# Kernel optimization log

Measured on AMD Instinct MI355X. Metric: run time of the kernel, lower is better.

Reference implementation:

```python
import jax, jax.numpy as jnp
import numpy as np
import math

B, L, D_IN, D, H, NL, FF = 8, 1024, 32, 512, 8, 6, 64
DK = D // H

def _ln(x, g, b, eps=1e-5):
    m = jnp.mean(x, axis=-1, keepdims=True)
    v = jnp.mean((x - m) ** 2, axis=-1, keepdims=True)
    return (x - m) * jax.lax.rsqrt(v + eps) * g + b

def setup_inputs() -> dict:
    key = jax.random.key(0)
    ks = jax.random.split(key, 32)
    def nrm(k, shape, s=0.02):
        return jax.random.normal(k, shape, jnp.float32) * s
    x = jax.random.normal(ks[0], (B, L, D_IN), jnp.float32)
    mask = jnp.broadcast_to(jnp.tril(jnp.ones((L, L), jnp.int32))[None], (B, L, L))
    obs_time = jnp.arange(B * L, dtype=jnp.float32).reshape(B, L)
    inp = {
        "x": x, "mask": mask, "obs_time": obs_time,
        # embedding MLP: Linear(d_input,d) -> ReLU -> [Dropout] -> LayerNorm -> Linear(d,d)
        "emb_w1": nrm(ks[1], (D_IN, D)), "emb_b1": jnp.zeros((D,), jnp.float32),
        "emb_g": jnp.ones((D,), jnp.float32), "emb_beta": jnp.zeros((D,), jnp.float32),
        "emb_w2": nrm(ks[2], (D, D)), "emb_b2": jnp.zeros((D,), jnp.float32),
        # per-layer stacked params [NL, ...]
        "wq": nrm(ks[3], (NL, D, D)), "wk": nrm(ks[4], (NL, D, D)), "wv": nrm(ks[5], (NL, D, D)),
        "wo": nrm(ks[6], (NL, D, D)), "bo": jnp.zeros((NL, D), jnp.float32),
        "fw1": nrm(ks[7], (NL, D, FF)), "fb1": jnp.zeros((NL, FF), jnp.float32),
        "fw2": nrm(ks[8], (NL, FF, D)), "fb2": jnp.zeros((NL, D), jnp.float32),
        "g1": jnp.ones((NL, D), jnp.float32), "b1": jnp.zeros((NL, D), jnp.float32),
        "g2": jnp.ones((NL, D), jnp.float32), "b2": jnp.zeros((NL, D), jnp.float32),
    }
    return inp

def reference(x, mask, obs_time, emb_w1, emb_b1, emb_g, emb_beta, emb_w2, emb_b2,
              wq, wk, wv, wo, bo, fw1, fb1, fw2, fb2, g1, b1, g2, b2):
    # positional encoding: pe[...,0::2]=sin(t*div), pe[...,1::2]=cos(t*div)
    t = obs_time[..., None]  # [B,L,1]
    div = jnp.exp(jnp.arange(0, D, 2, dtype=jnp.float32) * (-math.log(10000.0) / D))
    pe = jnp.stack([jnp.sin(t * div), jnp.cos(t * div)], axis=-1).reshape(x.shape[0], x.shape[1], D)

    # embedding MLP (dropout = identity at eval)
    h = jax.nn.relu(x @ emb_w1 + emb_b1)
    h = _ln(h, emb_g, emb_beta)
    h = h @ emb_w2 + emb_b2
    h = h + pe

    Bx, Lx = h.shape[0], h.shape[1]
    scale = 1.0 / np.sqrt(DK).astype(np.float32)
    mask4 = (mask == 0)[:, None]  # [B,1,L,L]
    for i in range(NL):
        # self-attention
        q = (h @ wq[i]).reshape(Bx, Lx, H, DK).transpose(0, 2, 1, 3)  # bhld
        k = (h @ wk[i]).reshape(Bx, Lx, H, DK).transpose(0, 2, 1, 3)
        v = (h @ wv[i]).reshape(Bx, Lx, H, DK).transpose(0, 2, 1, 3)
        scores = jnp.einsum('bhqd,bhkd->bhqk', q, k) * scale
        scores = jnp.where(mask4, -jnp.inf, scores)
        attn = jax.nn.softmax(scores, axis=-1)
        o = jnp.einsum('bhqk,bhkd->bhqd', attn, v).transpose(0, 2, 1, 3).reshape(Bx, Lx, D)
        o = o @ wo[i] + bo[i]
        h = _ln(h + o, g1[i], b1[i])
        # feed-forward d -> 64 -> d
        f = jax.nn.relu(h @ fw1[i] + fb1[i]) @ fw2[i] + fb2[i]
        h = _ln(h + f, g2[i], b2[i])
    return h
```

## Files before the change

kernel.cpp:

```cpp
#include <hip/hip_runtime.h>
#include <math.h>

typedef unsigned short u16;
typedef unsigned int   u32;
typedef __bf16 bf16_t;
typedef bf16_t bf16x8 __attribute__((ext_vector_type(8)));
typedef float  f32x4  __attribute__((ext_vector_type(4)));
typedef u16    u16x8  __attribute__((ext_vector_type(8)));
typedef u16    u16x4  __attribute__((ext_vector_type(4)));

#define B_   8
#define L_   1024
#define DIN_ 32
#define D_   512
#define H_   8
#define NL_  6
#define FF_  64
#define M_   (B_*L_)
#define DD_  (D_*D_)

#define PE_COEF (-0.017988946039015984f)
#define SC2     (0.18033688011112042f)

__device__ __forceinline__ u16 f2bf(float f) {
  u32 u = __builtin_bit_cast(u32, f);
  u32 r = (u + 0x7FFFu + ((u >> 16) & 1u)) >> 16;
  return (u16)r;
}
__device__ __forceinline__ u16 f2bf_fast(float f) {
  u32 u = __builtin_bit_cast(u32, f);
  return (u16)((u + 0x8000u) >> 16);
}
__device__ __forceinline__ float bf2f(u16 v) {
  u32 u = ((u32)v) << 16;
  return __builtin_bit_cast(float, u);
}

#define GLOAD_LDS16(gp, lp) \
  __builtin_amdgcn_global_load_lds((const __attribute__((address_space(1))) u32*)(gp), \
                                   (__attribute__((address_space(3))) u32*)(lp), 16, 0, 0)

__global__ __launch_bounds__(256) void transpose_all(const float* __restrict__ wq, const float* __restrict__ wk,
                                                     const float* __restrict__ wv, const float* __restrict__ wo,
                                                     const float* __restrict__ ew2,
                                                     u16* __restrict__ qkvt, u16* __restrict__ wot,
                                                     u16* __restrict__ ew2t) {
  __shared__ float tile[32][33];
  int z = blockIdx.z;
  const float* src;
  u16* dst;
  if (z < 18) {
    int grp = z / 6, i = z % 6;
    src = (grp == 0 ? wq : grp == 1 ? wk : wv) + (size_t)i*DD_;
    dst = qkvt + (size_t)i*3*DD_ + (size_t)grp*DD_;
  } else if (z < 24) {
    int i = z - 18;
    src = wo + (size_t)i*DD_;
    dst = wot + (size_t)i*DD_;
  } else {
    src = ew2; dst = ew2t;
  }
  int k0 = blockIdx.y * 32, n0 = blockIdx.x * 32;
  int tx = threadIdx.x & 31, ty = threadIdx.x >> 5;
  #pragma unroll
  for (int i = 0; i < 4; ++i)
    tile[ty + i*8][tx] = src[(size_t)(k0 + ty + i*8)*512 + n0 + tx];
  __syncthreads();
  #pragma unroll
  for (int i = 0; i < 4; ++i)
    dst[(size_t)(n0 + ty + i*8)*512 + k0 + tx] = f2bf(tile[tx][ty + i*8]);
}

__global__ __launch_bounds__(256) void transpose_k(const float* __restrict__ W, u16* __restrict__ Wt,
                                                   int K, int N, size_t in_zs, size_t out_zs) {
  __shared__ float tile[32][33];
  size_t mi = (size_t)blockIdx.z * in_zs;
  size_t mo = (size_t)blockIdx.z * out_zs;
  int k0 = blockIdx.y * 32, n0 = blockIdx.x * 32;
  int tx = threadIdx.x & 31, ty = threadIdx.x >> 5;
  #pragma unroll
  for (int i = 0; i < 4; ++i)
    tile[ty + i*8][tx] = W[mi + (size_t)(k0 + ty + i*8)*N + n0 + tx];
  __syncthreads();
  #pragma unroll
  for (int i = 0; i < 4; ++i)
    Wt[mo + (size_t)(n0 + ty + i*8)*K + k0 + tx] = f2bf(tile[tx][ty + i*8]);
}

__global__ __launch_bounds__(256) void emb1_ln_kernel(const float* __restrict__ x, const float* __restrict__ W1,
                               const float* __restrict__ b1, const float* __restrict__ g,
                               const float* __restrict__ beta, u16* __restrict__ outb) {
  __shared__ float xs[DIN_];
  __shared__ float red[4];
  int m = blockIdx.x;
  int tid = threadIdx.x;
  if (tid < DIN_) xs[tid] = x[m*DIN_ + tid];
  __syncthreads();
  float v[2];
  #pragma unroll
  for (int r = 0; r < 2; ++r) {
    int n = tid + r*256;
    float acc = b1[n];
    #pragma unroll
    for (int k = 0; k < DIN_; ++k) acc += xs[k] * W1[k*D_ + n];
    v[r] = fmaxf(acc, 0.f);
  }
  float s = v[0] + v[1];
  #pragma unroll
  for (int off = 32; off > 0; off >>= 1) s += __shfl_down(s, off, 64);
  int wid = tid >> 6;
  if ((tid & 63) == 0) red[wid] = s;
  __syncthreads();
  float mean = (red[0] + red[1] + red[2] + red[3]) * (1.f/D_);
  float d0 = v[0] - mean, d1 = v[1] - mean;
  float vv = d0*d0 + d1*d1;
  #pragma unroll
  for (int off = 32; off > 0; off >>= 1) vv += __shfl_down(vv, off, 64);
  __syncthreads();
  if ((tid & 63) == 0) red[wid] = vv;
  __syncthreads();
  float var = (red[0] + red[1] + red[2] + red[3]) * (1.f/D_);
  float rstd = rsqrtf(var + 1e-5f);
  outb[(size_t)m*D_ + tid]       = f2bf(d0*rstd*g[tid]       + beta[tid]);
  outb[(size_t)m*D_ + tid + 256] = f2bf(d1*rstd*g[tid + 256] + beta[tid + 256]);
}

__global__ __launch_bounds__(256) void add_ln_kernel(const float* __restrict__ hin, const u16* __restrict__ res,
                              const float* __restrict__ g, const float* __restrict__ b,
                              float* __restrict__ outf, u16* __restrict__ outb) {
  int w = threadIdx.x >> 6, lane = threadIdx.x & 63;
  int m = blockIdx.x * 4 + w;
  const float* hr = hin + (size_t)m*D_;
  const u16*   rr = res + (size_t)m*D_;
  float v[8];
  float s = 0.f;
  #pragma unroll
  for (int i = 0; i < 8; ++i) {
    int c = lane + i*64;
    v[i] = hr[c] + bf2f(rr[c]);
    s += v[i];
  }
  #pragma unroll
  for (int off = 32; off > 0; off >>= 1) s += __shfl_xor(s, off, 64);
  float mean = s * (1.f/D_);
  float vs = 0.f;
  #pragma unroll
  for (int i = 0; i < 8; ++i) { v[i] -= mean; vs += v[i]*v[i]; }
  #pragma unroll
  for (int off = 32; off > 0; off >>= 1) vs += __shfl_xor(vs, off, 64);
  float rstd = rsqrtf(vs * (1.f/D_) + 1e-5f);
  #pragma unroll
  for (int i = 0; i < 8; ++i) {
    int c = lane + i*64;
    float o = v[i]*rstd*g[c] + b[c];
    outf[(size_t)m*D_ + c] = o;
    outb[(size_t)m*D_ + c] = f2bf(o);
  }
}

template<int BM, int BN, int EPI, bool WF, bool WB>
__global__ __launch_bounds__(256) void mgemm(const u16* __restrict__ A, const u16* __restrict__ Bt,
                            const float* __restrict__ bias, const float* __restrict__ extra,
                            float* __restrict__ Cf, u16* __restrict__ Cb,
                            int M, int N, int K) {
  constexpr int BK = 64;
  constexpr int AI = BM/32, BI = BN/32;
  __shared__ __align__(16) u16 As[2][BM*BK];
  __shared__ __align__(16) u16 Bs[2][BN*BK];
  const int WR = BM/2, WC = BN/2, MR = WR/16, NR = WC/16;
  int nx = gridDim.x;
  int nwg = nx * gridDim.y;
  int flat = blockIdx.y * nx + blockIdx.x;
  int wid = (flat & 7) * (nwg >> 3) + (flat >> 3);
  int bm = (wid / nx) * BM, bn = (wid % nx) * BN;
  int tid = threadIdx.x, w = tid >> 6, l = tid & 63;
  int wr = w >> 1, wc = w & 1;
  int lq = l & 15, lg = l >> 4;
  int lrow8 = l >> 3, lcol8 = l & 7;
  f32x4 acc[MR][NR];
  #pragma unroll
  for (int m = 0; m < MR; ++m)
    #pragma unroll
    for (int n = 0; n < NR; ++n) acc[m][n] = f32x4{0.f,0.f,0.f,0.f};

  auto stage = [&](int t, int bi) {
    int k0 = t * BK;
    #pragma unroll
    for (int i = 0; i < AI; ++i) {
      int row = (i*4 + w)*8 + lrow8;
      int c8 = lcol8 ^ ((row & 1) << 2);
      GLOAD_LDS16(A + (size_t)(bm + row)*K + k0 + c8*8, &As[bi][(i*4 + w)*512]);
    }
    #pragma unroll
    for (int i = 0; i < BI; ++i) {
      int row = (i*4 + w)*8 + lrow8;
      int c8 = lcol8 ^ ((row & 1) << 2);
      GLOAD_LDS16(Bt + (size_t)(bn + row)*K + k0 + c8*8, &Bs[bi][(i*4 + w)*512]);
    }
  };

  int nk = K / BK;
  stage(0, 0);
  asm volatile("s_waitcnt vmcnt(0)" ::: "memory");
  __builtin_amdgcn_s_barrier();
  __builtin_amdgcn_sched_barrier(0);

  int xh = lq & 1;
  #pragma unroll 1
  for (int t = 0; t < nk; ++t) {
    int buf = t & 1;
    if (t + 1 < nk) stage(t + 1, buf ^ 1);
    bf16x8 af[MR][2], bf[NR][2];
    #pragma unroll
    for (int m = 0; m < MR; ++m)
      #pragma unroll
      for (int h = 0; h < 2; ++h)
        af[m][h] = *(const bf16x8*)&As[buf][(wr*WR + m*16 + lq)*BK + (h ^ xh)*32 + lg*8];
    #pragma unroll
    for (int n = 0; n < NR; ++n)
      #pragma unroll
      for (int h = 0; h < 2; ++h)
        bf[n][h] = *(const bf16x8*)&Bs[buf][(wc*WC + n*16 + lq)*BK + (h ^ xh)*32 + lg*8];
    #pragma unroll
    for (int m = 0; m < MR; ++m)
      #pragma unroll
      for (int n = 0; n < NR; ++n) {
        acc[m][n] = __builtin_amdgcn_mfma_f32_16x16x32_bf16(af[m][0], bf[n][0], acc[m][n], 0, 0, 0);
        acc[m][n] = __builtin_amdgcn_mfma_f32_16x16x32_bf16(af[m][1], bf[n][1], acc[m][n], 0, 0, 0);
      }
    if (t + 1 < nk) {
      asm volatile("s_waitcnt vmcnt(0)" ::: "memory");
      __builtin_amdgcn_s_barrier();
      __builtin_amdgcn_sched_barrier(0);
    }
  }

  #pragma unroll
  for (int m = 0; m < MR; ++m) {
    #pragma unroll
    for (int n = 0; n < NR; ++n) {
      #pragma unroll
      for (int r = 0; r < 4; ++r) {
        int row = bm + wr*WR + m*16 + lg*4 + r;
        int col = bn + wc*WC + n*16 + lq;
        float v = acc[m][n][r];
        if (EPI & 1) v += bias[col];
        if (EPI & 2) v = fmaxf(v, 0.f);
        if (EPI & 4) {
          float fr  = __expf((float)(col & ~1) * PE_COEF);
          float arg = extra[row] * fr;
          v += (col & 1) ? cosf(arg) : sinf(arg);
        }
        if (WF) Cf[(size_t)row*N + col] = v;
        if (WB) Cb[(size_t)row*N + col] = f2bf(v);
      }
    }
  }
}

#define QS_ 1536
__global__ __launch_bounds__(256) void attn_kernel(const u16* __restrict__ Q, const u16* __restrict__ Kp,
                                                   const u16* __restrict__ V, u16* __restrict__ O) {
  __shared__ __align__(16) u16 Ks[2][64*72];
  __shared__ __align__(16) u16 Vt[2][64*72];
  __shared__ __align__(16) u16 Ps[4][16*72];
  int flat = blockIdx.y * 8 + blockIdx.x;
  int wid  = (flat & 7) * 64 + (flat >> 3);
  int pair = wid & 7, bh = wid >> 3;
  int b = bh >> 3, hh = bh & 7;
  int rowbase = b * L_, col0 = hh * 64;
  int tid = threadIdx.x, w = tid >> 6, l = tid & 63;
  int lq = l & 15, lg = l >> 4;

  int krow = tid >> 3, kseg = tid & 7;
  int vg = tid >> 5, vd2 = (tid & 31) * 2;

  u16x8 kr0, kr1;
  u32 vr[8];
  u16x8 oc16;
  #pragma unroll
  for (int i = 0; i < 8; ++i) oc16[i] = 0x3F80u;
  const bf16x8 onesA = __builtin_bit_cast(bf16x8, oc16);

  #define LOADKV(t) { \
    kr0 = *(const u16x8*)&Kp[(size_t)(rowbase + (t)*64 + krow)*QS_ + col0 + kseg*8]; \
    kr1 = *(const u16x8*)&Kp[(size_t)(rowbase + (t)*64 + krow + 32)*QS_ + col0 + kseg*8]; \
    _Pragma("unroll") \
    for (int i_ = 0; i_ < 8; ++i_) \
      vr[i_] = *(const u32*)&V[(size_t)(rowbase + (t)*64 + vg*8 + i_)*QS_ + col0 + vd2]; }

  LOADKV(0);

  #pragma unroll 1
  for (int half = 0; half < 2; ++half) {
    int qt = half ? (15 - pair) : pair;
    int qrow = rowbase + qt*64 + w*16 + lq;
    bf16x8 qa0 = *(const bf16x8*)&Q[(size_t)qrow*QS_ + col0 + lg*8];
    bf16x8 qa1 = *(const bf16x8*)&Q[(size_t)qrow*QS_ + col0 + 32 + lg*8];
    float m_s[4];
    f32x4 o[4], o4;
    #pragma unroll
    for (int r = 0; r < 4; ++r) m_s[r] = -1e30f;
    #pragma unroll
    for (int n = 0; n < 4; ++n) o[n] = f32x4{0.f,0.f,0.f,0.f};
    o4 = f32x4{0.f,0.f,0.f,0.f};

    #pragma unroll 1
    for (int kt = 0; kt <= qt; ++kt) {
      int buf = kt & 1;
      __syncthreads();
      *(u16x8*)&Ks[buf][krow*72 + kseg*8]        = kr0;
      *(u16x8*)&Ks[buf][(krow + 32)*72 + kseg*8] = kr1;
      {
        u16x8 vlo, vhi;
        #pragma unroll
        for (int i = 0; i < 8; ++i) { vlo[i] = (u16)(vr[i] & 0xffffu); vhi[i] = (u16)(vr[i] >> 16); }
        *(u16x8*)&Vt[buf][vd2*72 + vg*8]     = vlo;
        *(u16x8*)&Vt[buf][(vd2+1)*72 + vg*8] = vhi;
      }
      __syncthreads();
      int nt = (kt < qt) ? (kt + 1) : (half == 0 ? 0 : -1);
      if (nt >= 0) LOADKV(nt);

      f32x4 t4[4];
      __builtin_amdgcn_s_setprio(1);
      #pragma unroll
      for (int f = 0; f < 4; ++f) {
        bf16x8 k0 = *(const bf16x8*)&Ks[buf][(f*16 + lq)*72 + lg*8];
        bf16x8 k1 = *(const bf16x8*)&Ks[buf][(f*16 + lq)*72 + 32 + lg*8];
        f32x4 z = f32x4{0.f,0.f,0.f,0.f};
        z = __builtin_amdgcn_mfma_f32_16x16x32_bf16(qa0, k0, z, 0, 0, 0);
        z = __builtin_amdgcn_mfma_f32_16x16x32_bf16(qa1, k1, z, 0, 0, 0);
        #pragma unroll
        for (int r = 0; r < 4; ++r) t4[f][r] = z[r] * SC2;
      }
      __builtin_amdgcn_s_setprio(0);
      if (kt == qt) {
        #pragma unroll
        for (int f = 0; f < 4; ++f) {
          int kvg = f*16 + lq;
          #pragma unroll
          for (int r = 0; r < 4; ++r)
            if (kvg > w*16 + lg*4 + r) t4[f][r] = -1e30f;
        }
      }
      float tm[4];
      bool need = false;
      #pragma unroll
      for (int r = 0; r < 4; ++r) {
        float v = fmaxf(fmaxf(t4[0][r], t4[1][r]), fmaxf(t4[2][r], t4[3][r]));
        v = fmaxf(v, __shfl_xor(v, 1));
        v = fmaxf(v, __shfl_xor(v, 2));
        v = fmaxf(v, __shfl_xor(v, 4));
        v = fmaxf(v, __shfl_xor(v, 8));
        tm[r] = v;
        need = need || (v > m_s[r]);
      }
      if (__any(need)) {
        float corr[4];
        #pragma unroll
        for (int r = 0; r < 4; ++r) {
          float mn = fmaxf(m_s[r], tm[r]);
          corr[r] = __builtin_amdgcn_exp2f(m_s[r] - mn);
          m_s[r] = mn;
        }
        int bsrc = (lq >> 2)*16 + lq;
        float c0 = __shfl(corr[0], bsrc);
        float c1 = __shfl(corr[1], bsrc);
        float c2 = __shfl(corr[2], bsrc);
        float c3 = __shfl(corr[3], bsrc);
        float cb = (lq & 2) ? ((lq & 1) ? c3 : c2) : ((lq & 1) ? c1 : c0);
        #pragma unroll
        for (int n = 0; n < 4; ++n)
          #pragma unroll
          for (int r = 0; r < 4; ++r) o[n][r] *= cb;
        #pragma unroll
        for (int r = 0; r < 4; ++r) o4[r] *= cb;
      }
      #pragma unroll
      for (int r = 0; r < 4; ++r) {
        int prow = (lg*4 + r)*72;
        Ps[w][prow + lq]      = f2bf_fast(__builtin_amdgcn_exp2f(t4[0][r] - m_s[r]));
        Ps[w][prow + 16 + lq] = f2bf_fast(__builtin_amdgcn_exp2f(t4[1][r] - m_s[r]));
        Ps[w][prow + 32 + lq] = f2bf_fast(__builtin_amdgcn_exp2f(t4[2][r] - m_s[r]));
        Ps[w][prow + 48 + lq] = f2bf_fast(__builtin_amdgcn_exp2f(t4[3][r] - m_s[r]));
      }
      bf16x8 pB0 = *(const bf16x8*)&Ps[w][lq*72 + lg*8];
      bf16x8 pB1 = *(const bf16x8*)&Ps[w][lq*72 + 32 + lg*8];
      __builtin_amdgcn_s_setprio(1);
      o4 = __builtin_amdgcn_mfma_f32_16x16x32_bf16(onesA, pB0, o4, 0, 0, 0);
      o4 = __builtin_amdgcn_mfma_f32_16x16x32_bf16(onesA, pB1, o4, 0, 0, 0);
      #pragma unroll
      for (int n = 0; n < 4; ++n) {
        bf16x8 vA0 = *(const bf16x8*)&Vt[buf][(n*16 + lq)*72 + lg*8];
        bf16x8 vA1 = *(const bf16x8*)&Vt[buf][(n*16 + lq)*72 + 32 + lg*8];
        o[n] = __builtin_amdgcn_mfma_f32_16x16x32_bf16(vA0, pB0, o[n], 0, 0, 0);
        o[n] = __builtin_amdgcn_mfma_f32_16x16x32_bf16(vA1, pB1, o[n], 0, 0, 0);
      }
      __builtin_amdgcn_s_setprio(0);
    }
    float inv = 1.f / o4[0];
    #pragma unroll
    for (int n = 0; n < 4; ++n) {
      u16x4 pk;
      #pragma unroll
      for (int r = 0; r < 4; ++r) pk[r] = f2bf(o[n][r] * inv);
      *(u16x4*)&O[(size_t)(rowbase + qt*64 + w*16 + lq)*D_ + col0 + n*16 + lg*4] = pk;
    }
  }
  #undef LOADKV
}

extern "C" void kernel_launch(void* const* d_in, const int* in_sizes, int n_in,
                              void* d_out, int out_size, void* d_ws, size_t ws_size,
                              hipStream_t stream) {
  (void)in_sizes; (void)n_in; (void)out_size; (void)ws_size;
  const float* x      = (const float*)d_in[0];
  const float* obs    = (const float*)d_in[2];
  const float* emb_w1 = (const float*)d_in[3];
  const float* emb_b1 = (const float*)d_in[4];
  const float* emb_g  = (const float*)d_in[5];
  const float* emb_be = (const float*)d_in[6];
  const float* emb_w2 = (const float*)d_in[7];
  const float* emb_b2 = (const float*)d_in[8];
  const float* wq  = (const float*)d_in[9];
  const float* wk  = (const float*)d_in[10];
  const float* wv  = (const float*)d_in[11];
  const float* wo  = (const float*)d_in[12];
  const float* bo  = (const float*)d_in[13];
  const float* fw1 = (const float*)d_in[14];
  const float* fb1 = (const float*)d_in[15];
  const float* fw2 = (const float*)d_in[16];
  const float* fb2 = (const float*)d_in[17];
  const float* g1  = (const float*)d_in[18];
  const float* b1  = (const float*)d_in[19];
  const float* g2  = (const float*)d_in[20];
  const float* b2  = (const float*)d_in[21];
  float* out = (float*)d_out;

  float* hf  = (float*)d_ws;
  u16* hb    = (u16*)(hf + (size_t)M_*D_);
  u16* qkvb  = hb + (size_t)M_*D_;
  u16* ob    = qkvb + (size_t)M_*3*D_;
  u16* ofb   = ob + (size_t)M_*D_;
  u16* fhb   = ofb + (size_t)M_*D_;
  u16* qkvt  = fhb + (size_t)M_*FF_;
  u16* wot   = qkvt + (size_t)18*DD_;
  u16* ew2t  = wot + (size_t)6*DD_;
  u16* fw1t  = ew2t + (size_t)DD_;
  u16* fw2t  = fw1t + (size_t)6*D_*FF_;

  transpose_all<<<dim3(16,16,25), 256, 0, stream>>>(wq, wk, wv, wo, emb_w2, qkvt, wot, ew2t);
  transpose_k<<<dim3(2,16,6),  256, 0, stream>>>(fw1, fw1t, 512,  64, (size_t)D_*FF_, (size_t)D_*FF_);
  transpose_k<<<dim3(16,2,6),  256, 0, stream>>>(fw2, fw2t,  64, 512, (size_t)D_*FF_, (size_t)D_*FF_);

  emb1_ln_kernel<<<M_, 256, 0, stream>>>(x, emb_w1, emb_b1, emb_g, emb_be, ob);
  mgemm<128,128,5,true,true><<<dim3(4,64), 256, 0, stream>>>(ob, ew2t, emb_b2, obs, hf, hb, M_, D_, D_);

  for (int i = 0; i < NL_; ++i) {
    mgemm<128,128,0,false,true><<<dim3(12,64), 256, 0, stream>>>(hb, qkvt + (size_t)i*3*DD_,
        nullptr, nullptr, nullptr, qkvb, M_, 3*D_, D_);
    attn_kernel<<<dim3(8, B_*H_), 256, 0, stream>>>(qkvb, qkvb + D_, qkvb + 2*D_, ob);
    mgemm<128,128,1,false,true><<<dim3(4,64), 256, 0, stream>>>(ob, wot + (size_t)i*DD_,
        bo + i*D_, nullptr, nullptr, ofb, M_, D_, D_);
    add_ln_kernel<<<M_/4, 256, 0, stream>>>(hf, ofb, g1 + i*D_, b1 + i*D_, hf, hb);
    mgemm<64,64,3,false,true><<<dim3(1,128), 256, 0, stream>>>(hb, fw1t + (size_t)i*D_*FF_,
        fb1 + i*FF_, nullptr, nullptr, fhb, M_, FF_, D_);
    mgemm<128,128,1,false,true><<<dim3(4,64), 256, 0, stream>>>(fhb, fw2t + (size_t)i*D_*FF_,
        fb2 + i*D_, nullptr, nullptr, ofb, M_, D_, FF_);
    add_ln_kernel<<<M_/4, 256, 0, stream>>>(hf, ofb, g2 + i*D_, b2 + i*D_,
        (i == NL_-1) ? out : hf, hb);
  }
}
```

Baseline: 866.7 us.

## Fuse FFN with residual LayerNorm, triple-buffer GEMM, and prefetch attention K/V

The FFN block's two GEMMs, ReLU, bias, residual add and LayerNorm are replaced by one fused kernel. Each block of it handles 32 rows, keeps the 64-wide hidden activation in LDS and reads the weights straight from global memory. The generic GEMM moves from a double-buffered BK=64 loop to a triple-buffered BK=32 pipeline with partial vmcnt waits, and the XOR swizzle is dropped. The attention kernel now writes the next K/V tile to LDS at the end of each iteration, removing one barrier per tile. Together these cut launches and the round trips for the FFN intermediate and its output, at the cost of possible LDS bank conflicts and lower weight reuse in the fused FFN.

```diff
diff --git a/kernel.cpp b/kernel.cpp
--- a/kernel.cpp
+++ b/kernel.cpp
@@ -163,10 +163,10 @@
                             const float* __restrict__ bias, const float* __restrict__ extra,
                             float* __restrict__ Cf, u16* __restrict__ Cb,
                             int M, int N, int K) {
-  constexpr int BK = 64;
-  constexpr int AI = BM/32, BI = BN/32;
-  __shared__ __align__(16) u16 As[2][BM*BK];
-  __shared__ __align__(16) u16 Bs[2][BN*BK];
+  constexpr int NBUF = 3;
+  constexpr int LPT = BM/64 + BN/64;
+  __shared__ __align__(16) u16 As[NBUF][BM*32];
+  __shared__ __align__(16) u16 Bs[NBUF][BN*32];
   const int WR = BM/2, WC = BN/2, MR = WR/16, NR = WC/16;
   int nx = gridDim.x;
   int nwg = nx * gridDim.y;
@@ -176,63 +176,58 @@
   int tid = threadIdx.x, w = tid >> 6, l = tid & 63;
   int wr = w >> 1, wc = w & 1;
   int lq = l & 15, lg = l >> 4;
-  int lrow8 = l >> 3, lcol8 = l & 7;
   f32x4 acc[MR][NR];
   #pragma unroll
   for (int m = 0; m < MR; ++m)
     #pragma unroll
     for (int n = 0; n < NR; ++n) acc[m][n] = f32x4{0.f,0.f,0.f,0.f};
 
+  int srow = w*16 + (l >> 2);
+  int scol = (l & 3)*8;
+
   auto stage = [&](int t, int bi) {
-    int k0 = t * BK;
-    #pragma unroll
-    for (int i = 0; i < AI; ++i) {
-      int row = (i*4 + w)*8 + lrow8;
-      int c8 = lcol8 ^ ((row & 1) << 2);
-      GLOAD_LDS16(A + (size_t)(bm + row)*K + k0 + c8*8, &As[bi][(i*4 + w)*512]);
-    }
-    #pragma unroll
-    for (int i = 0; i < BI; ++i) {
-      int row = (i*4 + w)*8 + lrow8;
-      int c8 = lcol8 ^ ((row & 1) << 2);
-      GLOAD_LDS16(Bt + (size_t)(bn + row)*K + k0 + c8*8, &Bs[bi][(i*4 + w)*512]);
-    }
+    int k0 = t << 5;
+    #pragma unroll
+    for (int i = 0; i < BM/64; ++i)
+      GLOAD_LDS16(A + (size_t)(bm + i*64 + srow)*K + k0 + scol, &As[bi][i*2048 + w*512]);
+    #pragma unroll
+    for (int i = 0; i < BN/64; ++i)
+      GLOAD_LDS16(Bt + (size_t)(bn + i*64 + srow)*K + k0 + scol, &Bs[bi][i*2048 + w*512]);
   };
 
-  int nk = K / BK;
+  int nk = K >> 5;
   stage(0, 0);
-  asm volatile("s_waitcnt vmcnt(0)" ::: "memory");
-  __builtin_amdgcn_s_barrier();
-  __builtin_amdgcn_sched_barrier(0);
-
-  int xh = lq & 1;
+  if (nk > 1) stage(1, 1);
+  int bi = 0;
   #pragma unroll 1
   for (int t = 0; t < nk; ++t) {
-    int buf = t & 1;
-    if (t + 1 < nk) stage(t + 1, buf ^ 1);
-    bf16x8 af[MR][2], bf[NR][2];
+    if (t + 1 < nk) {
+      if constexpr (LPT == 2)      asm volatile("s_waitcnt vmcnt(2)" ::: "memory");
+      else if constexpr (LPT == 3) asm volatile("s_waitcnt vmcnt(3)" ::: "memory");
+      else if constexpr (LPT == 4) asm volatile("s_waitcnt vmcnt(4)" ::: "memory");
+      else                         asm volatile("s_waitcnt vmcnt(0)" ::: "memory");
+    } else {
+      asm volatile("s_waitcnt vmcnt(0)" ::: "memory");
+    }
+    __builtin_amdgcn_s_barrier();
+    __builtin_amdgcn_sched_barrier(0);
+    if (t + 2 < nk) {
+      int b2 = bi + 2; if (b2 >= NBUF) b2 -= NBUF;
+      stage(t + 2, b2);
+    }
+    bf16x8 af[MR], bfr[NR];
     #pragma unroll
     for (int m = 0; m < MR; ++m)
-      #pragma unroll
-      for (int h = 0; h < 2; ++h)
-        af[m][h] = *(const bf16x8*)&As[buf][(wr*WR + m*16 + lq)*BK + (h ^ xh)*32 + lg*8];
+      af[m] = *(const bf16x8*)&As[bi][(wr*WR + m*16 + lq)*32 + lg*8];
     #pragma unroll
     for (int n = 0; n < NR; ++n)
-      #pragma unroll
-      for (int h = 0; h < 2; ++h)
-        bf[n][h] = *(const bf16x8*)&Bs[buf][(wc*WC + n*16 + lq)*BK + (h ^ xh)*32 + lg*8];
+      bfr[n] = *(const bf16x8*)&Bs[bi][(wc*WC + n*16 + lq)*32 + lg*8];
     #pragma unroll
     for (int m = 0; m < MR; ++m)
       #pragma unroll
-      for (int n = 0; n < NR; ++n) {
-        acc[m][n] = __builtin_amdgcn_mfma_f32_16x16x32_bf16(af[m][0], bf[n][0], acc[m][n], 0, 0, 0);
-        acc[m][n] = __builtin_amdgcn_mfma_f32_16x16x32_bf16(af[m][1], bf[n][1], acc[m][n], 0, 0, 0);
-      }
-    if (t + 1 < nk) {
-      asm volatile("s_waitcnt vmcnt(0)" ::: "memory");
-      __builtin_amdgcn_s_barrier();
-      __builtin_amdgcn_sched_barrier(0);
-    }
+      for (int n = 0; n < NR; ++n)
+        acc[m][n] = __builtin_amdgcn_mfma_f32_16x16x32_bf16(af[m], bfr[n], acc[m][n], 0, 0, 0);
+    bi = (bi + 1 == NBUF) ? 0 : bi + 1;
   }
 
   #pragma unroll
@@ -258,6 +253,117 @@
   }
 }
 
+__global__ __launch_bounds__(512) void ff_fused(const u16* __restrict__ Ain,
+        const u16* __restrict__ fw1t, const float* __restrict__ fb1,
+        const u16* __restrict__ fw2t, const float* __restrict__ fb2,
+        const float* __restrict__ hres, const float* __restrict__ g,
+        const float* __restrict__ bet, float* __restrict__ outf, u16* __restrict__ outb) {
+  __shared__ __align__(16) u16 Asw[32*512];
+  __shared__ __align__(16) u16 fls[32*72];
+  __shared__ float part[32][4];
+  int tid = threadIdx.x, w = tid >> 6, l = tid & 63;
+  int lq = l & 15, lg = l >> 4;
+  int bm = blockIdx.x * 32;
+  #pragma unroll
+  for (int i = 0; i < 4; ++i) {
+    int lam = tid + i*512;
+    int row = lam >> 6;
+    int slot = lam & 63;
+    int sslot = slot ^ (row & 7);
+    GLOAD_LDS16(Ain + (size_t)(bm + row)*512 + sslot*8, Asw + lam*8);
+  }
+  asm volatile("s_waitcnt vmcnt(0)" ::: "memory");
+  __syncthreads();
+  {
+    int mt = w >> 2, nt = w & 3;
+    f32x4 facc = f32x4{0.f,0.f,0.f,0.f};
+    const u16* bp = fw1t + (size_t)(nt*16 + lq)*512;
+    int arow = mt*16 + lq;
+    #pragma unroll
+    for (int ks = 0; ks < 16; ++ks) {
+      int slot = (ks*4 + lg) ^ (arow & 7);
+      bf16x8 a = *(const bf16x8*)&Asw[arow*512 + slot*8];
+      bf16x8 b = *(const bf16x8*)&bp[ks*32 + lg*8];
+      facc = __builtin_amdgcn_mfma_f32_16x16x32_bf16(a, b, facc, 0, 0, 0);
+    }
+    float bias = fb1[nt*16 + lq];
+    #pragma unroll
+    for (int r = 0; r < 4; ++r)
+      fls[(mt*16 + lg*4 + r)*72 + nt*16 + lq] = f2bf(fmaxf(facc[r] + bias, 0.f));
+  }
+  __syncthreads();
+  int m0 = (w >> 2) * 16;
+  int n0 = (w & 3) * 128;
+  f32x4 acc[8];
+  #pragma unroll
+  for (int n = 0; n < 8; ++n) acc[n] = f32x4{0.f,0.f,0.f,0.f};
+  #pragma unroll
+  for (int ks = 0; ks < 2; ++ks) {
+    bf16x8 a = *(const bf16x8*)&fls[(m0 + lq)*72 + ks*32 + lg*8];
+    #pragma unroll
+    for (int n = 0; n < 8; ++n) {
+      bf16x8 b = *(const bf16x8*)&fw2t[(size_t)(n0 + n*16 + lq)*64 + ks*32 + lg*8];
+      acc[n] = __builtin_amdgcn_mfma_f32_16x16x32_bf16(a, b, acc[n], 0, 0, 0);
+    }
+  }
+  float v[8][4];
+  float psum[4] = {0.f,0.f,0.f,0.f};
+  #pragma unroll
+  for (int n = 0; n < 8; ++n) {
+    int col = n0 + n*16 + lq;
+    float bias = fb2[col];
+    #pragma unroll
+    for (int r = 0; r < 4; ++r) {
+      int row = bm + m0 + lg*4 + r;
+      float t = acc[n][r] + bias + hres[(size_t)row*512 + col];
+      v[n][r] = t;
+      psum[r] += t;
+    }
+  }
+  #pragma unroll
+  for (int off = 1; off <= 8; off <<= 1)
+    #pragma unroll
+    for (int r = 0; r < 4; ++r) psum[r] += __shfl_xor(psum[r], off);
+  if (lq == 0)
+    #pragma unroll
+    for (int r = 0; r < 4; ++r) part[m0 + lg*4 + r][w & 3] = psum[r];
+  __syncthreads();
+  float mean[4];
+  #pragma unroll
+  for (int r = 0; r < 4; ++r) {
+    int row = m0 + lg*4 + r;
+    mean[r] = (part[row][0] + part[row][1] + part[row][2] + part[row][3]) * (1.f/512.f);
+  }
+  __syncthreads();
+  float pv[4] = {0.f,0.f,0.f,0.f};
+  #pragma unroll
+  for (int n = 0; n < 8; ++n)
+    #pragma unroll
+    for (int r = 0; r < 4; ++r) { v[n][r] -= mean[r]; pv[r] += v[n][r]*v[n][r]; }
+  #pragma unroll
+  for (int off = 1; off <= 8; off <<= 1)
+    #pragma unroll
+    for (int r = 0; r < 4; ++r) pv[r] += __shfl_xor(pv[r], off);
+  if (lq == 0)
+    #pragma unroll
+    for (int r = 0; r < 4; ++r) part[m0 + lg*4 + r][w & 3] = pv[r];
+  __syncthreads();
+  #pragma unroll
+  for (int r = 0; r < 4; ++r) {
+    int lrow = m0 + lg*4 + r;
+    float var = (part[lrow][0] + part[lrow][1] + part[lrow][2] + part[lrow][3]) * (1.f/512.f);
+    float rstd = rsqrtf(var + 1e-5f);
+    int row = bm + lrow;
+    #pragma unroll
+    for (int n = 0; n < 8; ++n) {
+      int col = n0 + n*16 + lq;
+      float o = v[n][r]*rstd*g[col] + bet[col];
+      outf[(size_t)row*512 + col] = o;
+      outb[(size_t)row*512 + col] = f2bf(o);
+    }
+  }
+}
+
 #define QS_ 1536
 __global__ __launch_bounds__(256) void attn_kernel(const u16* __restrict__ Q, const u16* __restrict__ Kp,
                                                    const u16* __restrict__ V, u16* __restrict__ O) {
@@ -289,6 +395,15 @@
     for (int i_ = 0; i_ < 8; ++i_) \
       vr[i_] = *(const u32*)&V[(size_t)(rowbase + (t)*64 + vg*8 + i_)*QS_ + col0 + vd2]; }
 
+  #define WRITE_LDS(bb) { \
+    *(u16x8*)&Ks[bb][krow*72 + kseg*8]        = kr0; \
+    *(u16x8*)&Ks[bb][(krow + 32)*72 + kseg*8] = kr1; \
+    u16x8 vlo, vhi; \
+    _Pragma("unroll") \
+    for (int i_ = 0; i_ < 8; ++i_) { vlo[i_] = (u16)(vr[i_] & 0xffffu); vhi[i_] = (u16)(vr[i_] >> 16); } \
+    *(u16x8*)&Vt[bb][vd2*72 + vg*8]     = vlo; \
+    *(u16x8*)&Vt[bb][(vd2+1)*72 + vg*8] = vhi; }
+
   LOADKV(0);
 
   #pragma unroll 1
@@ -305,19 +420,12 @@
     for (int n = 0; n < 4; ++n) o[n] = f32x4{0.f,0.f,0.f,0.f};
     o4 = f32x4{0.f,0.f,0.f,0.f};
 
+    __syncthreads();
+    WRITE_LDS(0);
+
     #pragma unroll 1
     for (int kt = 0; kt <= qt; ++kt) {
       int buf = kt & 1;
-      __syncthreads();
-      *(u16x8*)&Ks[buf][krow*72 + kseg*8]        = kr0;
-      *(u16x8*)&Ks[buf][(krow + 32)*72 + kseg*8] = kr1;
-      {
-        u16x8 vlo, vhi;
-        #pragma unroll
-        for (int i = 0; i < 8; ++i) { vlo[i] = (u16)(vr[i] & 0xffffu); vhi[i] = (u16)(vr[i] >> 16); }
-        *(u16x8*)&Vt[buf][vd2*72 + vg*8]     = vlo;
-        *(u16x8*)&Vt[buf][(vd2+1)*72 + vg*8] = vhi;
-      }
       __syncthreads();
       int nt = (kt < qt) ? (kt + 1) : (half == 0 ? 0 : -1);
       if (nt >= 0) LOADKV(nt);
@@ -348,13 +456,13 @@
       bool need = false;
       #pragma unroll
       for (int r = 0; r < 4; ++r) {
-        float v = fmaxf(fmaxf(t4[0][r], t4[1][r]), fmaxf(t4[2][r], t4[3][r]));
-        v = fmaxf(v, __shfl_xor(v, 1));
-        v = fmaxf(v, __shfl_xor(v, 2));
-        v = fmaxf(v, __shfl_xor(v, 4));
-        v = fmaxf(v, __shfl_xor(v, 8));
-        tm[r] = v;
-        need = need || (v > m_s[r]);
+        float vv = fmaxf(fmaxf(t4[0][r], t4[1][r]), fmaxf(t4[2][r], t4[3][r]));
+        vv = fmaxf(vv, __shfl_xor(vv, 1));
+        vv = fmaxf(vv, __shfl_xor(vv, 2));
+        vv = fmaxf(vv, __shfl_xor(vv, 4));
+        vv = fmaxf(vv, __shfl_xor(vv, 8));
+        tm[r] = vv;
+        need = need || (vv > m_s[r]);
       }
       if (__any(need)) {
         float corr[4];
@@ -398,6 +506,7 @@
         o[n] = __builtin_amdgcn_mfma_f32_16x16x32_bf16(vA1, pB1, o[n], 0, 0, 0);
       }
       __builtin_amdgcn_s_setprio(0);
+      if (kt < qt) WRITE_LDS(buf ^ 1);
     }
     float inv = 1.f / o4[0];
     #pragma unroll
@@ -409,6 +518,7 @@
     }
   }
   #undef LOADKV
+  #undef WRITE_LDS
 }
 
 extern "C" void kernel_launch(void* const* d_in, const int* in_sizes, int n_in,
@@ -443,8 +553,7 @@
   u16* qkvb  = hb + (size_t)M_*D_;
   u16* ob    = qkvb + (size_t)M_*3*D_;
   u16* ofb   = ob + (size_t)M_*D_;
-  u16* fhb   = ofb + (size_t)M_*D_;
-  u16* qkvt  = fhb + (size_t)M_*FF_;
+  u16* qkvt  = ofb + (size_t)M_*D_;
   u16* wot   = qkvt + (size_t)18*DD_;
   u16* ew2t  = wot + (size_t)6*DD_;
   u16* fw1t  = ew2t + (size_t)DD_;
@@ -464,11 +573,8 @@
     mgemm<128,128,1,false,true><<<dim3(4,64), 256, 0, stream>>>(ob, wot + (size_t)i*DD_,
         bo + i*D_, nullptr, nullptr, ofb, M_, D_, D_);
     add_ln_kernel<<<M_/4, 256, 0, stream>>>(hf, ofb, g1 + i*D_, b1 + i*D_, hf, hb);
-    mgemm<64,64,3,false,true><<<dim3(1,128), 256, 0, stream>>>(hb, fw1t + (size_t)i*D_*FF_,
-        fb1 + i*FF_, nullptr, nullptr, fhb, M_, FF_, D_);
-    mgemm<128,128,1,false,true><<<dim3(4,64), 256, 0, stream>>>(fhb, fw2t + (size_t)i*D_*FF_,
-        fb2 + i*D_, nullptr, nullptr, ofb, M_, D_, FF_);
-    add_ln_kernel<<<M_/4, 256, 0, stream>>>(hf, ofb, g2 + i*D_, b2 + i*D_,
+    ff_fused<<<M_/32, 512, 0, stream>>>(hb, fw1t + (size_t)i*D_*FF_, fb1 + i*FF_,
+        fw2t + (size_t)i*D_*FF_, fb2 + i*D_, hf, g2 + i*D_, b2 + i*D_,
         (i == NL_-1) ? out : hf, hb);
   }
 }
```

Measured after the change: 799.6 us. 1.08x faster.
